# Kernel optimization log

Measured on AMD Instinct MI355X. Metric: run time of the kernel, lower is better.

## Reference

```python
import jax, jax.numpy as jnp
import numpy as np

G, S, D, H = 32, 512, 128, 8   # num_groups, group_size, embed_dim, num_heads
HD = D // H                     # head_dim = 16
FFN = 2 * D                     # GLU hidden dim (ffn_dim = embed_dim * 2)
EPS = 1e-6


def _rmsnorm(x, w):
    return x * jax.lax.rsqrt(jnp.mean(x * x, axis=-1, keepdims=True) + EPS) * w


def setup_inputs() -> dict:
    key = jax.random.key(0)
    ks = jax.random.split(key, 12)
    BM = G * S
    s = 1.0 / float(np.sqrt(D))
    w = lambda k, shp, sc: (jax.random.normal(k, shp, jnp.float32) * sc)
    return {
        "x": jax.random.normal(ks[0], (BM, D), jnp.float32),
        "pe": jax.random.normal(ks[1], (BM, D), jnp.float32),
        "coords": jax.random.randint(ks[2], (BM, 4), 0, 128, jnp.int32),
        "Wq": w(ks[3], (D, D), s), "Wk": w(ks[4], (D, D), s),
        "Wv": w(ks[5], (D, D), s), "Wg": w(ks[6], (D, D), s),
        "Wo": w(ks[7], (D, D), s),
        "ln1_w": jnp.ones((D,), jnp.float32),
        "ln2_w": jnp.ones((D,), jnp.float32),
        "W_fc1": w(ks[8], (D, FFN), s),
        "W_gate": w(ks[9], (D, FFN), s),
        "W_fc2": w(ks[10], (FFN, D), 1.0 / float(np.sqrt(FFN))),
    }


def _decay_mask(coords):
    # coords: (BM,4) int; cols 1..3 are x,y,z voxel indices
    c = coords.reshape(G, S, 4)[..., 1:4].astype(jnp.float32)          # (G,S,3)
    dist = jnp.abs(c[:, :, None, :] - c[:, None, :, :]).sum(-1)        # (G,S,S) Manhattan
    decay = jnp.log(1.0 - 2.0 ** (-5.0 - jnp.arange(H, dtype=jnp.float32)))  # (H,)
    m = jnp.exp(dist[None] * decay[:, None, None, None])               # (H,G,S,S)
    m = jnp.nan_to_num(m)
    m = m / jnp.sqrt(m.sum(-1, keepdims=True))
    return jnp.transpose(m, (1, 0, 2, 3))                              # (G,H,S,S)


def reference(x, pe, coords, Wq, Wk, Wv, Wg, Wo, ln1_w, ln2_w, W_fc1, W_gate, W_fc2):
    mask = _decay_mask(coords)                                         # (G,H,S,S)

    # --- retention block (pre-norm) ---
    residual = x
    xn = _rmsnorm(x, ln1_w).reshape(G, S, D)
    qin = xn + pe.reshape(G, S, D)

    heads = lambda t: t.reshape(G, S, H, HD).transpose(0, 2, 1, 3)     # (G,H,S,HD)
    q = heads(qin @ Wq) * (HD ** -0.5)
    k = heads(qin @ Wk)
    v = heads(xn @ Wv)
    g = xn @ Wg                                                        # (G,S,D)

    qk = jnp.einsum('ghsd,ghtd->ghst', q, k)                           # (G,H,S,S)
    attn = jax.nn.softmax(qk, axis=-1) * mask
    denom = jnp.clip(jax.lax.stop_gradient(jnp.abs(attn).sum(-1, keepdims=True)), 1.0, None)
    attn = attn / denom
    o = jnp.einsum('ghst,ghtd->ghsd', attn, v)                         # (G,H,S,HD)
    # per-head RMSNorm (no affine), as group_norm over head_dim
    o = o * jax.lax.rsqrt(jnp.mean(o * o, axis=-1, keepdims=True) + EPS)
    o = o.transpose(0, 2, 1, 3).reshape(G, S, D)
    o = jax.nn.silu(g) * o                                             # swish output gate
    o = (o @ Wo).reshape(G * S, D)
    x1 = residual + o

    # --- GLU FFN block (pre-norm) ---
    h = _rmsnorm(x1, ln2_w)
    h = jax.nn.gelu(h @ W_fc1) * (h @ W_gate)
    return x1 + h @ W_fc2
```

## Files before the change

kernel.cpp:

```cpp
#include <hip/hip_runtime.h>

#define G_ 32
#define S_ 512
#define D_ 128
#define H_ 8
#define BM_ (G_*S_)
#define EPSF 1e-6f
#define VP_ 520

typedef float f32x4  __attribute__((ext_vector_type(4)));
typedef float f32x16 __attribute__((ext_vector_type(16)));
typedef short s16x8  __attribute__((ext_vector_type(8)));

typedef unsigned int uint32;

#if __has_builtin(__builtin_amdgcn_exp2f)
#define EXP2F(x) __builtin_amdgcn_exp2f(x)
#else
#define EXP2F(x) exp2f(x)
#endif

static __device__ __forceinline__ unsigned short f2bf(float f){
  uint32 u = __float_as_uint(f);
  u = (u + 0x7fffu + ((u >> 16) & 1u)) >> 16;
  return (unsigned short)u;
}
static __device__ __forceinline__ float bf2f(unsigned short h){
  return __uint_as_float(((uint32)h) << 16);
}
static __device__ __forceinline__ float siluf(float x){
  float e = EXP2F(-x * 1.4426950408889634f);
  return x / (1.0f + e);
}
static __device__ __forceinline__ float geluf(float x){
  float y = 0.7978845608028654f * (x + 0.044715f * x * x * x);
  y = fminf(fmaxf(y, -40.0f), 40.0f);
  float e = EXP2F(y * 2.8853900817779268f);
  float th = (e - 1.0f) / (e + 1.0f);
  return 0.5f * x * (1.0f + th);
}
static __device__ __forceinline__ uint32 sad3(uint32 a, uint32 b){
#if __has_builtin(__builtin_amdgcn_sad_u8)
  return __builtin_amdgcn_sad_u8(a, b, 0u);
#else
  uint32 d; uint32 z = 0;
  asm("v_sad_u8 %0, %1, %2, %3" : "=v"(d) : "v"(a), "v"(b), "v"(z));
  return d;
#endif
}

__global__ __launch_bounds__(256) void k_wprep_all(
    const float* __restrict__ w0, const float* __restrict__ w1,
    const float* __restrict__ w2, const float* __restrict__ w3,
    const float* __restrict__ w4, const float* __restrict__ w5,
    const float* __restrict__ w6, const float* __restrict__ w7,
    unsigned short* __restrict__ o0, unsigned short* __restrict__ o1,
    unsigned short* __restrict__ o2, unsigned short* __restrict__ o3,
    unsigned short* __restrict__ o4, unsigned short* __restrict__ o5,
    unsigned short* __restrict__ o6, unsigned short* __restrict__ o7){
  const int which = blockIdx.y;
  const float* W; unsigned short* O; int Kd, Nd;
  switch (which){
    case 0: W = w0; O = o0; Kd = 128; Nd = 128; break;
    case 1: W = w1; O = o1; Kd = 128; Nd = 128; break;
    case 2: W = w2; O = o2; Kd = 128; Nd = 128; break;
    case 3: W = w3; O = o3; Kd = 128; Nd = 128; break;
    case 4: W = w4; O = o4; Kd = 128; Nd = 128; break;
    case 5: W = w5; O = o5; Kd = 128; Nd = 256; break;
    case 6: W = w6; O = o6; Kd = 128; Nd = 256; break;
    default: W = w7; O = o7; Kd = 256; Nd = 128; break;
  }
  const int id = blockIdx.x * 256 + threadIdx.x;
  if (id >= Kd * Nd) return;
  const int n = id / Kd, k = id - n * Kd;
  O[id] = f2bf(W[(size_t)k * Nd + n]);
}

template<bool WITH_PE>
__global__ __launch_bounds__(256) void k_rms(const float* __restrict__ x,
    const float* __restrict__ pe, const float* __restrict__ w,
    unsigned short* __restrict__ xnb, unsigned short* __restrict__ qinb){
  const int lane = threadIdx.x & 63, wave = threadIdx.x >> 6;
  const int row = blockIdx.x * 4 + wave;
  const size_t base = (size_t)row * 128 + lane * 2;
  const float2 xv = *(const float2*)&x[base];
  float ss = xv.x * xv.x + xv.y * xv.y;
  #pragma unroll
  for (int off = 1; off < 64; off <<= 1) ss += __shfl_xor(ss, off, 64);
  const float rs = rsqrtf(ss * (1.0f / 128.0f) + EPSF);
  const float2 wv = *(const float2*)&w[lane * 2];
  const float a = xv.x * rs * wv.x, b = xv.y * rs * wv.y;
  ushort2 o; o.x = f2bf(a); o.y = f2bf(b);
  *(ushort2*)&xnb[base] = o;
  if (WITH_PE){
    const float2 pv = *(const float2*)&pe[base];
    ushort2 q; q.x = f2bf(a + pv.x); q.y = f2bf(b + pv.y);
    *(ushort2*)&qinb[base] = q;
  }
}

__global__ __launch_bounds__(512) void k_qkvg(
    const unsigned short* __restrict__ qinb, const unsigned short* __restrict__ xnb,
    const unsigned short* __restrict__ wqt, const unsigned short* __restrict__ wkt,
    const unsigned short* __restrict__ wvt, const unsigned short* __restrict__ wgt,
    unsigned short* __restrict__ qbf, unsigned short* __restrict__ kbf,
    unsigned short* __restrict__ vbf, unsigned short* __restrict__ gbf){
  __shared__ unsigned short wt[128 * 136];
  const int which = blockIdx.y;
  const unsigned short* WT = (which == 0) ? wqt : (which == 1) ? wkt : (which == 2) ? wvt : wgt;
  const unsigned short* A  = (which < 2) ? qinb : xnb;
  unsigned short* out      = (which == 0) ? qbf : (which == 1) ? kbf : (which == 2) ? vbf : gbf;
  const float scale = (which == 0) ? 0.36067376022224085f : 1.0f;
  const int tid = threadIdx.x;
  #pragma unroll
  for (int c = 0; c < 4; ++c){
    const int id8 = c * 512 + tid;
    const int n = id8 >> 4, k8 = id8 & 15;
    *(uint4*)&wt[n * 136 + k8 * 8] = *(const uint4*)&WT[n * 128 + k8 * 8];
  }
  const int lane = tid & 63, wave = tid >> 6;
  const int lr = lane & 15, lh = lane >> 4;
  const int rowbase = blockIdx.x * 128 + wave * 16;
  s16x8 af[4];
  const unsigned short* arow = A + (size_t)(rowbase + lr) * 128 + lh * 8;
  #pragma unroll
  for (int kc = 0; kc < 4; ++kc) af[kc] = *(const s16x8*)(arow + kc * 32);
  __syncthreads();
  #pragma unroll
  for (int ct = 0; ct < 8; ++ct){
    f32x4 acc = (f32x4)(0.0f);
    #pragma unroll
    for (int kc = 0; kc < 4; ++kc)
      acc = __builtin_amdgcn_mfma_f32_16x16x32_bf16(af[kc],
              *(const s16x8*)&wt[(ct * 16 + lr) * 136 + kc * 32 + lh * 8], acc, 0, 0, 0);
    #pragma unroll
    for (int j = 0; j < 4; ++j){
      const int row = rowbase + lh * 4 + j;
      const int col = ct * 16 + lr;
      out[(size_t)row * 128 + col] = f2bf(acc[j] * scale);
    }
  }
}

__global__ __launch_bounds__(256, 4) void k_attn(const unsigned short* __restrict__ qb,
    const unsigned short* __restrict__ kb, const unsigned short* __restrict__ vb,
    const int* __restrict__ coords, unsigned short* __restrict__ ob){
  __shared__ unsigned short kl[S_ * 16];
  __shared__ unsigned short vlT[16 * VP_];
  __shared__ uint32 cl1[S_];
  const int bx = blockIdx.x;
  const int g = bx >> 5, head = (bx >> 2) & 7, qtile = bx & 3;
  const int tid = threadIdx.x;
  const size_t rb = (size_t)g * S_ * 128 + head * 16;
  #pragma unroll
  for (int r = tid; r < S_; r += 256){
    const uint4* ksrc = (const uint4*)(kb + rb + (size_t)r * 128);
    ((uint4*)&kl[r * 16])[0] = ksrc[0];
    ((uint4*)&kl[r * 16])[1] = ksrc[1];
    const int4 cc = ((const int4*)coords)[g * S_ + r];
    cl1[r] = (uint32)(cc.y & 127) | ((uint32)(cc.z & 127) << 8) | ((uint32)(cc.w & 127) << 16);
  }
  {
    const int r0 = tid * 2;
    const unsigned short* v0 = vb + rb + (size_t)r0 * 128;
    const uint4 a0 = ((const uint4*)v0)[0], a1 = ((const uint4*)v0)[1];
    const uint4 b0 = ((const uint4*)(v0 + 128))[0], b1 = ((const uint4*)(v0 + 128))[1];
    const unsigned short* pa0 = (const unsigned short*)&a0;
    const unsigned short* pa1 = (const unsigned short*)&a1;
    const unsigned short* pb0 = (const unsigned short*)&b0;
    const unsigned short* pb1 = (const unsigned short*)&b1;
    #pragma unroll
    for (int hd = 0; hd < 8; ++hd){
      *(uint32*)&vlT[hd * VP_ + r0] = (uint32)pa0[hd] | ((uint32)pb0[hd] << 16);
      *(uint32*)&vlT[(hd + 8) * VP_ + r0] = (uint32)pa1[hd] | ((uint32)pb1[hd] << 16);
    }
  }
  __syncthreads();
  const int lane = tid & 63, wave = tid >> 6;
  const int lq = lane & 31, half = lane >> 5;
  const int qrow = qtile * 128 + wave * 32 + lq;
  const float decay2 = log2f(1.0f - EXP2F(-(float)(5 + head)));
  const s16x8 bq = *(const s16x8*)(qb + rb + (size_t)qrow * 128 + half * 8);
  const uint32 cs = cl1[qrow];
  f32x16 accO = (f32x16)(0.0f);
  float Z = 0.f, M = 0.f;
  const int vrow = (lq & 15) * VP_;
  for (int tc = 0; tc < 16; ++tc){
    const s16x8 ak = *(const s16x8*)&kl[(tc * 32 + lq) * 16 + half * 8];
    const uint4 cq0 = *(const uint4*)&cl1[tc * 32 + 4 * half];
    const uint4 cq1 = *(const uint4*)&cl1[tc * 32 + 8 + 4 * half];
    const uint4 cq2 = *(const uint4*)&cl1[tc * 32 + 16 + 4 * half];
    const uint4 cq3 = *(const uint4*)&cl1[tc * 32 + 24 + 4 * half];
    const f32x16 c = __builtin_amdgcn_mfma_f32_32x32x16_bf16(ak, bq, (f32x16)(0.0f), 0, 0, 0);
    float wv[16];
    #pragma unroll
    for (int i = 0; i < 16; ++i){
      const uint4& cq = (i < 4) ? cq0 : (i < 8) ? cq1 : (i < 12) ? cq2 : cq3;
      const uint32 ct1 = (&cq.x)[i & 3];
      const uint32 dist = sad3(cs, ct1);
      const float e2 = EXP2F((float)dist * decay2);
      const float e1 = EXP2F(c[i]);
      wv[i] = e1 * e2;
      Z += e1; M += e2;
    }
    union { uint32 u[4]; s16x8 v; } f0, f1;
    #pragma unroll
    for (int j = 0; j < 4; ++j){
      asm("v_cvt_pk_bf16_f32 %0, %1, %2" : "=v"(f0.u[j]) : "v"(wv[2 * j]), "v"(wv[2 * j + 1]));
      asm("v_cvt_pk_bf16_f32 %0, %1, %2" : "=v"(f1.u[j]) : "v"(wv[8 + 2 * j]), "v"(wv[9 + 2 * j]));
    }
    const int vcol = tc * 32 + 4 * half;
    union { uint32 u[4]; s16x8 v; } bv0, bv1;
    *(uint2*)&bv0.u[0] = *(const uint2*)&vlT[vrow + vcol];
    *(uint2*)&bv0.u[2] = *(const uint2*)&vlT[vrow + vcol + 8];
    *(uint2*)&bv1.u[0] = *(const uint2*)&vlT[vrow + vcol + 16];
    *(uint2*)&bv1.u[2] = *(const uint2*)&vlT[vrow + vcol + 24];
    accO = __builtin_amdgcn_mfma_f32_32x32x16_bf16(f0.v, bv0.v, accO, 0, 0, 0);
    accO = __builtin_amdgcn_mfma_f32_32x32x16_bf16(f1.v, bv1.v, accO, 0, 0, 0);
  }
  Z += __shfl_xor(Z, 32, 64);
  M += __shfl_xor(M, 32, 64);
  const float sc = Z * sqrtf(M);
  const float epsp = EPSF * sc * sc;
  const size_t qbase = (size_t)(g * S_ + qtile * 128 + wave * 32);
  #pragma unroll
  for (int i = 0; i < 16; ++i){
    const int r = (i & 3) + 8 * (i >> 2) + 4 * half;
    const float v = accO[i];
    float ss = v * v;
    ss += __shfl_xor(ss, 1, 64); ss += __shfl_xor(ss, 2, 64);
    ss += __shfl_xor(ss, 4, 64); ss += __shfl_xor(ss, 8, 64);
    const float ei = __shfl(epsp, r, 64);
    const float on = v * rsqrtf(ss * 0.0625f + ei);
    if (lq < 16)
      ob[(qbase + r) * 128 + head * 16 + lq] = f2bf(on);
  }
}

__global__ __launch_bounds__(256) void k_wo(const unsigned short* __restrict__ g,
    const unsigned short* __restrict__ o, const unsigned short* __restrict__ WT,
    const float* __restrict__ resid, float* __restrict__ outp){
  __shared__ unsigned short wt[64 * 136];
  const int y = blockIdx.y;
  const int tid = threadIdx.x;
  #pragma unroll
  for (int c = 0; c < 4; ++c){
    const int id8 = c * 256 + tid;
    const int n = id8 >> 4, k8 = id8 & 15;
    *(uint4*)&wt[n * 136 + k8 * 8] = *(const uint4*)&WT[(size_t)(y * 64 + n) * 128 + k8 * 8];
  }
  const int lane = tid & 63, wave = tid >> 6;
  const int lr = lane & 15, lh = lane >> 4;
  const int rowbase = blockIdx.x * 64 + wave * 16;
  s16x8 af[4];
  const size_t abase = (size_t)(rowbase + lr) * 128 + lh * 8;
  #pragma unroll
  for (int kc = 0; kc < 4; ++kc){
    const s16x8 gv = *(const s16x8*)(g + abase + kc * 32);
    const s16x8 ov = *(const s16x8*)(o + abase + kc * 32);
    s16x8 r;
    #pragma unroll
    for (int j = 0; j < 8; ++j)
      r[j] = (short)f2bf(siluf(bf2f((unsigned short)gv[j])) * bf2f((unsigned short)ov[j]));
    af[kc] = r;
  }
  __syncthreads();
  #pragma unroll
  for (int ct = 0; ct < 4; ++ct){
    f32x4 acc = (f32x4)(0.0f);
    #pragma unroll
    for (int kc = 0; kc < 4; ++kc)
      acc = __builtin_amdgcn_mfma_f32_16x16x32_bf16(af[kc],
              *(const s16x8*)&wt[(ct * 16 + lr) * 136 + kc * 32 + lh * 8], acc, 0, 0, 0);
    #pragma unroll
    for (int j = 0; j < 4; ++j){
      const int row = rowbase + lh * 4 + j;
      const int col = y * 64 + ct * 16 + lr;
      const size_t idx = (size_t)row * 128 + col;
      outp[idx] = acc[j] + resid[idx];
    }
  }
}

__global__ __launch_bounds__(256) void k_dual(const unsigned short* __restrict__ A,
    const unsigned short* __restrict__ W1T, const unsigned short* __restrict__ W2T,
    unsigned short* __restrict__ hh){
  __shared__ unsigned short w1l[128 * 136];
  __shared__ unsigned short w2l[128 * 136];
  const int y = blockIdx.y;
  const int tid = threadIdx.x;
  #pragma unroll
  for (int c = 0; c < 8; ++c){
    const int id8 = c * 256 + tid;
    const int n = id8 >> 4, k8 = id8 & 15;
    *(uint4*)&w1l[n * 136 + k8 * 8] = *(const uint4*)&W1T[(size_t)(y * 128 + n) * 128 + k8 * 8];
    *(uint4*)&w2l[n * 136 + k8 * 8] = *(const uint4*)&W2T[(size_t)(y * 128 + n) * 128 + k8 * 8];
  }
  const int lane = tid & 63, wave = tid >> 6;
  const int lr = lane & 15, lh = lane >> 4;
  const int rowbase = blockIdx.x * 64 + wave * 16;
  s16x8 af[4];
  const unsigned short* arow = A + (size_t)(rowbase + lr) * 128 + lh * 8;
  #pragma unroll
  for (int kc = 0; kc < 4; ++kc) af[kc] = *(const s16x8*)(arow + kc * 32);
  __syncthreads();
  #pragma unroll
  for (int ct = 0; ct < 8; ++ct){
    f32x4 a1 = (f32x4)(0.0f), a2 = (f32x4)(0.0f);
    #pragma unroll
    for (int kc = 0; kc < 4; ++kc){
      a1 = __builtin_amdgcn_mfma_f32_16x16x32_bf16(af[kc],
             *(const s16x8*)&w1l[(ct * 16 + lr) * 136 + kc * 32 + lh * 8], a1, 0, 0, 0);
      a2 = __builtin_amdgcn_mfma_f32_16x16x32_bf16(af[kc],
             *(const s16x8*)&w2l[(ct * 16 + lr) * 136 + kc * 32 + lh * 8], a2, 0, 0, 0);
    }
    #pragma unroll
    for (int j = 0; j < 4; ++j){
      const int row = rowbase + lh * 4 + j;
      const int col = y * 128 + ct * 16 + lr;
      hh[(size_t)row * 256 + col] = f2bf(geluf(a1[j]) * a2[j]);
    }
  }
}

__global__ __launch_bounds__(256) void k_fc2(const unsigned short* __restrict__ hh,
    const unsigned short* __restrict__ WT, const float* __restrict__ x1,
    float* __restrict__ outp){
  __shared__ unsigned short wt[64 * 264];
  const int y = blockIdx.y;
  const int tid = threadIdx.x;
  #pragma unroll
  for (int c = 0; c < 8; ++c){
    const int id8 = c * 256 + tid;
    const int n = id8 >> 5, k8 = id8 & 31;
    *(uint4*)&wt[n * 264 + k8 * 8] = *(const uint4*)&WT[(size_t)(y * 64 + n) * 256 + k8 * 8];
  }
  const int lane = tid & 63, wave = tid >> 6;
  const int lr = lane & 15, lh = lane >> 4;
  const int rowbase = blockIdx.x * 64 + wave * 16;
  s16x8 af[8];
  const unsigned short* arow = hh + (size_t)(rowbase + lr) * 256 + lh * 8;
  #pragma unroll
  for (int kc = 0; kc < 8; ++kc) af[kc] = *(const s16x8*)(arow + kc * 32);
  __syncthreads();
  #pragma unroll
  for (int ct = 0; ct < 4; ++ct){
    f32x4 acc = (f32x4)(0.0f);
    #pragma unroll
    for (int kc = 0; kc < 8; ++kc)
      acc = __builtin_amdgcn_mfma_f32_16x16x32_bf16(af[kc],
              *(const s16x8*)&wt[(ct * 16 + lr) * 264 + kc * 32 + lh * 8], acc, 0, 0, 0);
    #pragma unroll
    for (int j = 0; j < 4; ++j){
      const int row = rowbase + lh * 4 + j;
      const int col = y * 64 + ct * 16 + lr;
      const size_t idx = (size_t)row * 128 + col;
      outp[idx] = acc[j] + x1[idx];
    }
  }
}

extern "C" void kernel_launch(void* const* d_in, const int* in_sizes, int n_in,
                              void* d_out, int out_size, void* d_ws, size_t ws_size,
                              hipStream_t stream){
  const float* x     = (const float*)d_in[0];
  const float* pe    = (const float*)d_in[1];
  const int*   coords= (const int*)d_in[2];
  const float* Wq    = (const float*)d_in[3];
  const float* Wk    = (const float*)d_in[4];
  const float* Wv    = (const float*)d_in[5];
  const float* Wg    = (const float*)d_in[6];
  const float* Wo    = (const float*)d_in[7];
  const float* ln1   = (const float*)d_in[8];
  const float* ln2   = (const float*)d_in[9];
  const float* Wfc1  = (const float*)d_in[10];
  const float* Wgate = (const float*)d_in[11];
  const float* Wfc2  = (const float*)d_in[12];
  float* out = (float*)d_out;
  char* ws = (char*)d_ws;

  const size_t SZB = 4194304;
  unsigned short* xnb  = (unsigned short*)(ws);
  unsigned short* qinb = (unsigned short*)(ws + 1 * SZB);
  unsigned short* qbf  = (unsigned short*)(ws + 2 * SZB);
  unsigned short* kbf  = (unsigned short*)(ws + 3 * SZB);
  unsigned short* vbf  = (unsigned short*)(ws + 4 * SZB);
  unsigned short* gbf  = (unsigned short*)(ws + 5 * SZB);
  unsigned short* obf  = (unsigned short*)(ws + 6 * SZB);
  float*          x1   = (float*)(ws + 7 * SZB);
  char* wbase = ws + 7 * SZB + 8388608;
  unsigned short* wqt   = (unsigned short*)(wbase);
  unsigned short* wkt   = (unsigned short*)(wbase + 32768);
  unsigned short* wvt   = (unsigned short*)(wbase + 65536);
  unsigned short* wgt   = (unsigned short*)(wbase + 98304);
  unsigned short* wot   = (unsigned short*)(wbase + 131072);
  unsigned short* fc1t  = (unsigned short*)(wbase + 163840);
  unsigned short* gatet = (unsigned short*)(wbase + 229376);
  unsigned short* fc2t  = (unsigned short*)(wbase + 294912);
  unsigned short* hnb = xnb;
  unsigned short* hhb = qbf;

  dim3 b256(256);
  k_wprep_all<<<dim3(128, 8), b256, 0, stream>>>(Wq, Wk, Wv, Wg, Wo, Wfc1, Wgate, Wfc2,
                                                 wqt, wkt, wvt, wgt, wot, fc1t, gatet, fc2t);
  k_rms<true><<<4096, b256, 0, stream>>>(x, pe, ln1, xnb, qinb);
  k_qkvg<<<dim3(128, 4), dim3(512), 0, stream>>>(qinb, xnb, wqt, wkt, wvt, wgt,
                                                 qbf, kbf, vbf, gbf);
  k_attn<<<1024, b256, 0, stream>>>(qbf, kbf, vbf, coords, obf);
  k_wo<<<dim3(256, 2), b256, 0, stream>>>(gbf, obf, wot, x, x1);
  k_rms<false><<<4096, b256, 0, stream>>>(x1, nullptr, ln2, hnb, nullptr);
  k_dual<<<dim3(256, 2), b256, 0, stream>>>(hnb, fc1t, gatet, hhb);
  k_fc2<<<dim3(256, 2), b256, 0, stream>>>(hhb, fc2t, x1, out);
}
```

Baseline: 87.67 us.

## Fuse RMSNorm into QKVG and FFN GEMM kernels and compact weight prep grid

```diff
diff --git a/kernel.cpp b/kernel.cpp
--- a/kernel.cpp
+++ b/kernel.cpp
@@ -6,7 +6,7 @@
 #define H_ 8
 #define BM_ (G_*S_)
 #define EPSF 1e-6f
-#define VP_ 520
+#define VP_ 516
 
 typedef float f32x4  __attribute__((ext_vector_type(4)));
 typedef float f32x16 __attribute__((ext_vector_type(16)));
@@ -58,49 +58,24 @@
     unsigned short* __restrict__ o2, unsigned short* __restrict__ o3,
     unsigned short* __restrict__ o4, unsigned short* __restrict__ o5,
     unsigned short* __restrict__ o6, unsigned short* __restrict__ o7){
-  const int which = blockIdx.y;
-  const float* W; unsigned short* O; int Kd, Nd;
-  switch (which){
-    case 0: W = w0; O = o0; Kd = 128; Nd = 128; break;
-    case 1: W = w1; O = o1; Kd = 128; Nd = 128; break;
-    case 2: W = w2; O = o2; Kd = 128; Nd = 128; break;
-    case 3: W = w3; O = o3; Kd = 128; Nd = 128; break;
-    case 4: W = w4; O = o4; Kd = 128; Nd = 128; break;
-    case 5: W = w5; O = o5; Kd = 128; Nd = 256; break;
-    case 6: W = w6; O = o6; Kd = 128; Nd = 256; break;
-    default: W = w7; O = o7; Kd = 256; Nd = 128; break;
-  }
   const int id = blockIdx.x * 256 + threadIdx.x;
-  if (id >= Kd * Nd) return;
-  const int n = id / Kd, k = id - n * Kd;
-  O[id] = f2bf(W[(size_t)k * Nd + n]);
-}
-
-template<bool WITH_PE>
-__global__ __launch_bounds__(256) void k_rms(const float* __restrict__ x,
-    const float* __restrict__ pe, const float* __restrict__ w,
-    unsigned short* __restrict__ xnb, unsigned short* __restrict__ qinb){
-  const int lane = threadIdx.x & 63, wave = threadIdx.x >> 6;
-  const int row = blockIdx.x * 4 + wave;
-  const size_t base = (size_t)row * 128 + lane * 2;
-  const float2 xv = *(const float2*)&x[base];
-  float ss = xv.x * xv.x + xv.y * xv.y;
-  #pragma unroll
-  for (int off = 1; off < 64; off <<= 1) ss += __shfl_xor(ss, off, 64);
-  const float rs = rsqrtf(ss * (1.0f / 128.0f) + EPSF);
-  const float2 wv = *(const float2*)&w[lane * 2];
-  const float a = xv.x * rs * wv.x, b = xv.y * rs * wv.y;
-  ushort2 o; o.x = f2bf(a); o.y = f2bf(b);
-  *(ushort2*)&xnb[base] = o;
-  if (WITH_PE){
-    const float2 pv = *(const float2*)&pe[base];
-    ushort2 q; q.x = f2bf(a + pv.x); q.y = f2bf(b + pv.y);
-    *(ushort2*)&qinb[base] = q;
-  }
+  const float* W; unsigned short* O; int Kd, Nd, lid;
+  if (id < 81920){
+    const int which = id >> 14;
+    W = (which == 0) ? w0 : (which == 1) ? w1 : (which == 2) ? w2 : (which == 3) ? w3 : w4;
+    O = (which == 0) ? o0 : (which == 1) ? o1 : (which == 2) ? o2 : (which == 3) ? o3 : o4;
+    Kd = 128; Nd = 128; lid = id & 16383;
+  } else if (id < 114688){ W = w5; O = o5; Kd = 128; Nd = 256; lid = id - 81920; }
+  else if (id < 147456){   W = w6; O = o6; Kd = 128; Nd = 256; lid = id - 114688; }
+  else if (id < 180224){   W = w7; O = o7; Kd = 256; Nd = 128; lid = id - 147456; }
+  else return;
+  const int n = lid / Kd, k = lid - n * Kd;
+  O[lid] = f2bf(W[(size_t)k * Nd + n]);
 }
 
 __global__ __launch_bounds__(512) void k_qkvg(
-    const unsigned short* __restrict__ qinb, const unsigned short* __restrict__ xnb,
+    const float* __restrict__ x, const float* __restrict__ pe,
+    const float* __restrict__ ln1,
     const unsigned short* __restrict__ wqt, const unsigned short* __restrict__ wkt,
     const unsigned short* __restrict__ wvt, const unsigned short* __restrict__ wgt,
     unsigned short* __restrict__ qbf, unsigned short* __restrict__ kbf,
@@ -108,7 +83,6 @@
   __shared__ unsigned short wt[128 * 136];
   const int which = blockIdx.y;
   const unsigned short* WT = (which == 0) ? wqt : (which == 1) ? wkt : (which == 2) ? wvt : wgt;
-  const unsigned short* A  = (which < 2) ? qinb : xnb;
   unsigned short* out      = (which == 0) ? qbf : (which == 1) ? kbf : (which == 2) ? vbf : gbf;
   const float scale = (which == 0) ? 0.36067376022224085f : 1.0f;
   const int tid = threadIdx.x;
@@ -121,10 +95,41 @@
   const int lane = tid & 63, wave = tid >> 6;
   const int lr = lane & 15, lh = lane >> 4;
   const int rowbase = blockIdx.x * 128 + wave * 16;
+  const size_t xb = (size_t)(rowbase + lr) * 128 + lh * 8;
+  float xv[32];
+  float ss = 0.f;
+  #pragma unroll
+  for (int kc = 0; kc < 4; ++kc){
+    const float4 a = *(const float4*)&x[xb + kc * 32];
+    const float4 b = *(const float4*)&x[xb + kc * 32 + 4];
+    xv[kc*8+0]=a.x; xv[kc*8+1]=a.y; xv[kc*8+2]=a.z; xv[kc*8+3]=a.w;
+    xv[kc*8+4]=b.x; xv[kc*8+5]=b.y; xv[kc*8+6]=b.z; xv[kc*8+7]=b.w;
+    ss += a.x*a.x + a.y*a.y + a.z*a.z + a.w*a.w;
+    ss += b.x*b.x + b.y*b.y + b.z*b.z + b.w*b.w;
+  }
+  ss += __shfl_xor(ss, 16, 64);
+  ss += __shfl_xor(ss, 32, 64);
+  const float rs = rsqrtf(ss * (1.0f / 128.0f) + EPSF);
   s16x8 af[4];
-  const unsigned short* arow = A + (size_t)(rowbase + lr) * 128 + lh * 8;
-  #pragma unroll
-  for (int kc = 0; kc < 4; ++kc) af[kc] = *(const s16x8*)(arow + kc * 32);
+  #pragma unroll
+  for (int kc = 0; kc < 4; ++kc){
+    const float4 w0 = *(const float4*)&ln1[kc * 32 + lh * 8];
+    const float4 w1 = *(const float4*)&ln1[kc * 32 + lh * 8 + 4];
+    float n0 = xv[kc*8+0]*rs*w0.x, n1 = xv[kc*8+1]*rs*w0.y;
+    float n2 = xv[kc*8+2]*rs*w0.z, n3 = xv[kc*8+3]*rs*w0.w;
+    float n4 = xv[kc*8+4]*rs*w1.x, n5 = xv[kc*8+5]*rs*w1.y;
+    float n6 = xv[kc*8+6]*rs*w1.z, n7 = xv[kc*8+7]*rs*w1.w;
+    if (which < 2){
+      const float4 p0 = *(const float4*)&pe[xb + kc * 32];
+      const float4 p1 = *(const float4*)&pe[xb + kc * 32 + 4];
+      n0 += p0.x; n1 += p0.y; n2 += p0.z; n3 += p0.w;
+      n4 += p1.x; n5 += p1.y; n6 += p1.z; n7 += p1.w;
+    }
+    s16x8 r;
+    r[0]=(short)f2bf(n0); r[1]=(short)f2bf(n1); r[2]=(short)f2bf(n2); r[3]=(short)f2bf(n3);
+    r[4]=(short)f2bf(n4); r[5]=(short)f2bf(n5); r[6]=(short)f2bf(n6); r[7]=(short)f2bf(n7);
+    af[kc] = r;
+  }
   __syncthreads();
   #pragma unroll
   for (int ct = 0; ct < 8; ++ct){
@@ -152,6 +157,10 @@
   const int g = bx >> 5, head = (bx >> 2) & 7, qtile = bx & 3;
   const int tid = threadIdx.x;
   const size_t rb = (size_t)g * S_ * 128 + head * 16;
+  const int lane = tid & 63, wave = tid >> 6;
+  const int lq = lane & 31, half = lane >> 5;
+  const int qrow = qtile * 128 + wave * 32 + lq;
+  const s16x8 bq = *(const s16x8*)(qb + rb + (size_t)qrow * 128 + half * 8);
   #pragma unroll
   for (int r = tid; r < S_; r += 256){
     const uint4* ksrc = (const uint4*)(kb + rb + (size_t)r * 128);
@@ -176,14 +185,10 @@
     }
   }
   __syncthreads();
-  const int lane = tid & 63, wave = tid >> 6;
-  const int lq = lane & 31, half = lane >> 5;
-  const int qrow = qtile * 128 + wave * 32 + lq;
   const float decay2 = log2f(1.0f - EXP2F(-(float)(5 + head)));
-  const s16x8 bq = *(const s16x8*)(qb + rb + (size_t)qrow * 128 + half * 8);
   const uint32 cs = cl1[qrow];
   f32x16 accO = (f32x16)(0.0f);
-  float Z = 0.f, M = 0.f;
+  float2 zm0 = {0.f,0.f}, zm1 = {0.f,0.f}, zm2 = {0.f,0.f}, zm3 = {0.f,0.f};
   const int vrow = (lq & 15) * VP_;
   for (int tc = 0; tc < 16; ++tc){
     const s16x8 ak = *(const s16x8*)&kl[(tc * 32 + lq) * 16 + half * 8];
@@ -201,7 +206,8 @@
       const float e2 = EXP2F((float)dist * decay2);
       const float e1 = EXP2F(c[i]);
       wv[i] = e1 * e2;
-      Z += e1; M += e2;
+      float2& zm = (i & 2) ? ((i & 1) ? zm3 : zm2) : ((i & 1) ? zm1 : zm0);
+      zm.x += e1; zm.y += e2;
     }
     union { uint32 u[4]; s16x8 v; } f0, f1;
     #pragma unroll
@@ -218,6 +224,8 @@
     accO = __builtin_amdgcn_mfma_f32_32x32x16_bf16(f0.v, bv0.v, accO, 0, 0, 0);
     accO = __builtin_amdgcn_mfma_f32_32x32x16_bf16(f1.v, bv1.v, accO, 0, 0, 0);
   }
+  float Z = (zm0.x + zm1.x) + (zm2.x + zm3.x);
+  float M = (zm0.y + zm1.y) + (zm2.y + zm3.y);
   Z += __shfl_xor(Z, 32, 64);
   M += __shfl_xor(M, 32, 64);
   const float sc = Z * sqrtf(M);
@@ -282,7 +290,8 @@
   }
 }
 
-__global__ __launch_bounds__(256) void k_dual(const unsigned short* __restrict__ A,
+__global__ __launch_bounds__(256) void k_dual(const float* __restrict__ x1,
+    const float* __restrict__ ln2,
     const unsigned short* __restrict__ W1T, const unsigned short* __restrict__ W2T,
     unsigned short* __restrict__ hh){
   __shared__ unsigned short w1l[128 * 136];
@@ -299,10 +308,33 @@
   const int lane = tid & 63, wave = tid >> 6;
   const int lr = lane & 15, lh = lane >> 4;
   const int rowbase = blockIdx.x * 64 + wave * 16;
+  const size_t xb = (size_t)(rowbase + lr) * 128 + lh * 8;
+  float xv[32];
+  float ss = 0.f;
+  #pragma unroll
+  for (int kc = 0; kc < 4; ++kc){
+    const float4 a = *(const float4*)&x1[xb + kc * 32];
+    const float4 b = *(const float4*)&x1[xb + kc * 32 + 4];
+    xv[kc*8+0]=a.x; xv[kc*8+1]=a.y; xv[kc*8+2]=a.z; xv[kc*8+3]=a.w;
+    xv[kc*8+4]=b.x; xv[kc*8+5]=b.y; xv[kc*8+6]=b.z; xv[kc*8+7]=b.w;
+    ss += a.x*a.x + a.y*a.y + a.z*a.z + a.w*a.w;
+    ss += b.x*b.x + b.y*b.y + b.z*b.z + b.w*b.w;
+  }
+  ss += __shfl_xor(ss, 16, 64);
+  ss += __shfl_xor(ss, 32, 64);
+  const float rs = rsqrtf(ss * (1.0f / 128.0f) + EPSF);
   s16x8 af[4];
-  const unsigned short* arow = A + (size_t)(rowbase + lr) * 128 + lh * 8;
-  #pragma unroll
-  for (int kc = 0; kc < 4; ++kc) af[kc] = *(const s16x8*)(arow + kc * 32);
+  #pragma unroll
+  for (int kc = 0; kc < 4; ++kc){
+    const float4 w0 = *(const float4*)&ln2[kc * 32 + lh * 8];
+    const float4 w1 = *(const float4*)&ln2[kc * 32 + lh * 8 + 4];
+    s16x8 r;
+    r[0]=(short)f2bf(xv[kc*8+0]*rs*w0.x); r[1]=(short)f2bf(xv[kc*8+1]*rs*w0.y);
+    r[2]=(short)f2bf(xv[kc*8+2]*rs*w0.z); r[3]=(short)f2bf(xv[kc*8+3]*rs*w0.w);
+    r[4]=(short)f2bf(xv[kc*8+4]*rs*w1.x); r[5]=(short)f2bf(xv[kc*8+5]*rs*w1.y);
+    r[6]=(short)f2bf(xv[kc*8+6]*rs*w1.z); r[7]=(short)f2bf(xv[kc*8+7]*rs*w1.w);
+    af[kc] = r;
+  }
   __syncthreads();
   #pragma unroll
   for (int ct = 0; ct < 8; ++ct){
@@ -380,15 +412,14 @@
   char* ws = (char*)d_ws;
 
   const size_t SZB = 4194304;
-  unsigned short* xnb  = (unsigned short*)(ws);
-  unsigned short* qinb = (unsigned short*)(ws + 1 * SZB);
-  unsigned short* qbf  = (unsigned short*)(ws + 2 * SZB);
-  unsigned short* kbf  = (unsigned short*)(ws + 3 * SZB);
-  unsigned short* vbf  = (unsigned short*)(ws + 4 * SZB);
-  unsigned short* gbf  = (unsigned short*)(ws + 5 * SZB);
-  unsigned short* obf  = (unsigned short*)(ws + 6 * SZB);
-  float*          x1   = (float*)(ws + 7 * SZB);
-  char* wbase = ws + 7 * SZB + 8388608;
+  unsigned short* qbf  = (unsigned short*)(ws);
+  unsigned short* kbf  = (unsigned short*)(ws + 1 * SZB);
+  unsigned short* vbf  = (unsigned short*)(ws + 2 * SZB);
+  unsigned short* gbf  = (unsigned short*)(ws + 3 * SZB);
+  unsigned short* obf  = (unsigned short*)(ws + 4 * SZB);
+  float*          x1   = (float*)(ws + 5 * SZB);
+  unsigned short* hhb  = (unsigned short*)(ws + 5 * SZB + 8388608);
+  char* wbase = ws + 5 * SZB + 2 * 8388608;
   unsigned short* wqt   = (unsigned short*)(wbase);
   unsigned short* wkt   = (unsigned short*)(wbase + 32768);
   unsigned short* wvt   = (unsigned short*)(wbase + 65536);
@@ -397,18 +428,14 @@
   unsigned short* fc1t  = (unsigned short*)(wbase + 163840);
   unsigned short* gatet = (unsigned short*)(wbase + 229376);
   unsigned short* fc2t  = (unsigned short*)(wbase + 294912);
-  unsigned short* hnb = xnb;
-  unsigned short* hhb = qbf;
 
   dim3 b256(256);
-  k_wprep_all<<<dim3(128, 8), b256, 0, stream>>>(Wq, Wk, Wv, Wg, Wo, Wfc1, Wgate, Wfc2,
-                                                 wqt, wkt, wvt, wgt, wot, fc1t, gatet, fc2t);
-  k_rms<true><<<4096, b256, 0, stream>>>(x, pe, ln1, xnb, qinb);
-  k_qkvg<<<dim3(128, 4), dim3(512), 0, stream>>>(qinb, xnb, wqt, wkt, wvt, wgt,
+  k_wprep_all<<<704, b256, 0, stream>>>(Wq, Wk, Wv, Wg, Wo, Wfc1, Wgate, Wfc2,
+                                        wqt, wkt, wvt, wgt, wot, fc1t, gatet, fc2t);
+  k_qkvg<<<dim3(128, 4), dim3(512), 0, stream>>>(x, pe, ln1, wqt, wkt, wvt, wgt,
                                                  qbf, kbf, vbf, gbf);
   k_attn<<<1024, b256, 0, stream>>>(qbf, kbf, vbf, coords, obf);
   k_wo<<<dim3(256, 2), b256, 0, stream>>>(gbf, obf, wot, x, x1);
-  k_rms<false><<<4096, b256, 0, stream>>>(x1, nullptr, ln2, hnb, nullptr);
-  k_dual<<<dim3(256, 2), b256, 0, stream>>>(hnb, fc1t, gatet, hhb);
+  k_dual<<<dim3(256, 2), b256, 0, stream>>>(x1, ln2, fc1t, gatet, hhb);
   k_fc2<<<dim3(256, 2), b256, 0, stream>>>(hhb, fc2t, x1, out);
 }
```

New measurement: 83.24 us. 5.1% less time.
